# Kernel optimization log

Hardware: AMD Instinct MI355X
Metric: run time of the kernel (lower is better)

The kernel has to match this reference:

```python
import jax, jax.numpy as jnp
import numpy as np

HIDDEN = 2048
HEAD_DIM = 128
GROUPS = 8
HEADS = HIDDEN // HEAD_DIM          # 16
HPG = HEADS // GROUPS               # heads per group = 2


def setup_inputs() -> dict:
    key = jax.random.key(0)
    ks = jax.random.split(key, 9)
    b, sl, sk = 2, 2048, 2048
    s = 0.02
    return {
        "q": jax.random.normal(ks[0], (b, sl, HIDDEN), jnp.float32),
        "k": jax.random.normal(ks[1], (b, sk, HIDDEN), jnp.float32),
        "v": jax.random.normal(ks[2], (b, sk, HIDDEN), jnp.float32),
        "Wq": jax.random.normal(ks[3], (HIDDEN, HIDDEN), jnp.float32) * s,
        "bq": jax.random.normal(ks[4], (HIDDEN,), jnp.float32) * s,
        "Wk": jax.random.normal(ks[5], (HIDDEN, HEAD_DIM * GROUPS), jnp.float32) * s,
        "bk": jax.random.normal(ks[6], (HEAD_DIM * GROUPS,), jnp.float32) * s,
        "Wv": jax.random.normal(ks[7], (HIDDEN, HEAD_DIM * GROUPS), jnp.float32) * s,
        "bv": jax.random.normal(ks[8], (HEAD_DIM * GROUPS,), jnp.float32) * s,
    }


def reference(q, k, v, Wq, bq, Wk, bk, Wv, bv):
    b, sl, _ = q.shape
    sk = k.shape[1]
    qp = q @ Wq + bq                                   # [b, sl, hidden]
    kp = k @ Wk + bk                                   # [b, sk, G*d]
    vp = v @ Wv + bv                                   # [b, sk, G*d]
    # head h = g*HPG + j uses group g, matching torch repeat_interleave on dim=1
    qh = qp.reshape(b, sl, GROUPS, HPG, HEAD_DIM).transpose(0, 2, 3, 1, 4)  # [b,G,hpg,sl,d]
    kh = kp.reshape(b, sk, GROUPS, HEAD_DIM).transpose(0, 2, 1, 3)          # [b,G,sk,d]
    vh = vp.reshape(b, sk, GROUPS, HEAD_DIM).transpose(0, 2, 1, 3)          # [b,G,sk,d]
    scale = 1.0 / jnp.sqrt(jnp.asarray(HEAD_DIM, qh.dtype))
    score = jnp.einsum("bghld,bgsd->bghls", qh, kh) * scale                 # [b,G,hpg,sl,sk]
    attn = jax.nn.softmax(score, axis=-1)
    out = jnp.einsum("bghls,bgsd->bghld", attn, vh)                         # [b,G,hpg,sl,d]
    out = out.transpose(0, 3, 1, 2, 4).reshape(b, sl, HIDDEN)
    return out
```

## Files before the change

### kernel.cpp

```cpp
#include <hip/hip_runtime.h>

typedef unsigned short u16;
typedef short v8s __attribute__((ext_vector_type(8)));
typedef float v4f __attribute__((ext_vector_type(4)));
typedef float v16f __attribute__((ext_vector_type(16)));

typedef __attribute__((address_space(3))) u16* lptr_t;
typedef const __attribute__((address_space(1))) void* gptr_t;

__device__ __forceinline__ u16 f2b(float f) {
  unsigned int u = __float_as_uint(f);
  u += 0x7fff + ((u >> 16) & 1);
  return (u16)(u >> 16);
}

__global__ __launch_bounds__(256) void prep_all(const float* __restrict__ q,
                                                const float* __restrict__ k,
                                                const float* __restrict__ v,
                                                const float* __restrict__ Wq,
                                                const float* __restrict__ Wk,
                                                const float* __restrict__ Wv,
                                                u16* __restrict__ qd,
                                                u16* __restrict__ kd,
                                                u16* __restrict__ vd,
                                                u16* __restrict__ wt) {
  __shared__ u16 tile[64][65];
  int blk = blockIdx.x;
  if (blk < 12288) {
    const float* s; u16* d;
    if (blk < 4096)      { s = q; d = qd; }
    else if (blk < 8192) { s = k; d = kd; blk -= 4096; }
    else                 { s = v; d = vd; blk -= 8192; }
    int i = (blk * 256 + threadIdx.x) * 8;
    float4 a = *(const float4*)&s[i];
    float4 b = *(const float4*)&s[i + 4];
    union { uint4 v4; u16 u[8]; } p;
    p.u[0] = f2b(a.x); p.u[1] = f2b(a.y); p.u[2] = f2b(a.z); p.u[3] = f2b(a.w);
    p.u[4] = f2b(b.x); p.u[5] = f2b(b.y); p.u[6] = f2b(b.z); p.u[7] = f2b(b.w);
    *(uint4*)&d[i] = p.v4;
    return;
  }
  blk -= 12288;
  const float* W; int N; u16* dst;
  if (blk < 1024)      { W = Wq; N = 2048; dst = wt; }
  else if (blk < 1536) { W = Wk; N = 1024; dst = wt + (size_t)2048 * 2048; blk -= 1024; }
  else                 { W = Wv; N = 1024; dst = wt + (size_t)3072 * 2048; blk -= 1536; }
  const int k0 = (blk & 31) * 64;
  const int n0 = (blk >> 5) * 64;
  const int t = threadIdx.x;
#pragma unroll
  for (int i = 0; i < 2; ++i) {
    int chunk = i * 256 + t;
    int kr = chunk >> 3;
    int nc = (chunk & 7) * 8;
    float4 a = *(const float4*)&W[(size_t)(k0 + kr) * N + n0 + nc];
    float4 b = *(const float4*)&W[(size_t)(k0 + kr) * N + n0 + nc + 4];
    tile[kr][nc + 0] = f2b(a.x); tile[kr][nc + 1] = f2b(a.y);
    tile[kr][nc + 2] = f2b(a.z); tile[kr][nc + 3] = f2b(a.w);
    tile[kr][nc + 4] = f2b(b.x); tile[kr][nc + 5] = f2b(b.y);
    tile[kr][nc + 6] = f2b(b.z); tile[kr][nc + 7] = f2b(b.w);
  }
  __syncthreads();
#pragma unroll
  for (int i = 0; i < 2; ++i) {
    int chunk = i * 256 + t;
    int nr = chunk >> 3;
    int kc = (chunk & 7) * 8;
    union { uint4 v; u16 u[8]; } cv;
#pragma unroll
    for (int j = 0; j < 8; ++j) cv.u[j] = tile[kc + j][nr];
    *(uint4*)&dst[(size_t)(n0 + nr) * 2048 + k0 + kc] = cv.v;
  }
}

__global__ __launch_bounds__(512, 2) void qkv_gemm8(const u16* __restrict__ qbf,
                                                    const u16* __restrict__ kbf,
                                                    const u16* __restrict__ vbf,
                                                    const u16* __restrict__ wt_all,
                                                    const float* __restrict__ bq,
                                                    const float* __restrict__ bk,
                                                    const float* __restrict__ bv,
                                                    u16* __restrict__ qp,
                                                    u16* __restrict__ kp,
                                                    u16* __restrict__ vpt) {
  __shared__ __align__(16) u16 A_sh[2][16384];
  __shared__ __align__(16) u16 B_sh[2][16384];

  const int bid = blockIdx.x;
  const int wg = (bid & 7) * 32 + (bid >> 3);
  const int m0 = (wg >> 4) * 256;
  const int n0 = (wg & 15) * 256;

  const int t = threadIdx.x;
  const int w = t >> 6, lane = t & 63;
  const int quad = lane >> 4, l16 = lane & 15;
  const int wr = w >> 2, wc = w & 3;

  const u16* Abase; const float* bias; int region, nloc0;
  if (n0 < 2048)      { Abase = qbf; bias = bq; region = 0; nloc0 = n0; }
  else if (n0 < 3072) { Abase = kbf; bias = bk; region = 1; nloc0 = n0 - 2048; }
  else                { Abase = vbf; bias = bv; region = 2; nloc0 = n0 - 3072; }

  const u16* GA = Abase + (size_t)m0 * 2048;
  const u16* GB = wt_all + (size_t)n0 * 2048;

  int offA[2][2], ldsA[2][2], offB[2][2], ldsB[2][2];
#pragma unroll
  for (int s_ = 0; s_ < 2; ++s_)
#pragma unroll
    for (int j = 0; j < 2; ++j) {
      int r0a = j * 128 + s_ * 64 + w * 8;
      int ra = r0a + (lane >> 3);
      offA[s_][j] = ra * 2048 + (((lane & 7) ^ (ra & 7)) << 3);
      ldsA[s_][j] = r0a * 64 + lane * 8;
      int r0b = j * 128 + s_ * 32 + (w >> 2) * 64 + (w & 3) * 8;
      int rb = r0b + (lane >> 3);
      offB[s_][j] = rb * 2048 + (((lane & 7) ^ (rb & 7)) << 3);
      ldsB[s_][j] = r0b * 64 + lane * 8;
    }

  int colR[2];
#pragma unroll
  for (int kk = 0; kk < 2; ++kk)
    colR[kk] = ((kk * 4 + quad) ^ (l16 & 7)) << 3;

#define ST_A(BUF, KEL, S_)                                                              \
  do {                                                                                  \
    _Pragma("unroll") for (int j_ = 0; j_ < 2; ++j_) {                                  \
      const u16* g_ = GA + (KEL) + offA[S_][j_];                                        \
      lptr_t l_ = (lptr_t)&A_sh[BUF][ldsA[S_][j_]];                                     \
      __builtin_amdgcn_global_load_lds((gptr_t)g_,                                      \
                                       (__attribute__((address_space(3))) void*)l_,     \
                                       16, 0, 0);                                       \
    }                                                                                   \
  } while (0)

#define ST_B(BUF, KEL, S_)                                                              \
  do {                                                                                  \
    _Pragma("unroll") for (int j_ = 0; j_ < 2; ++j_) {                                  \
      const u16* g_ = GB + (KEL) + offB[S_][j_];                                        \
      lptr_t l_ = (lptr_t)&B_sh[BUF][ldsB[S_][j_]];                                     \
      __builtin_amdgcn_global_load_lds((gptr_t)g_,                                      \
                                       (__attribute__((address_space(3))) void*)l_,     \
                                       16, 0, 0);                                       \
    }                                                                                   \
  } while (0)

#define RD_A(BUF, MS, DST)                                                              \
  do {                                                                                  \
    const int rb_ = wr * 128 + (MS) * 64;                                               \
    _Pragma("unroll") for (int m_ = 0; m_ < 4; ++m_)                                    \
    _Pragma("unroll") for (int kk_ = 0; kk_ < 2; ++kk_)                                 \
      DST[m_][kk_] = *(const v8s*)&A_sh[BUF][(rb_ + m_ * 16 + l16) * 64 + colR[kk_]];   \
  } while (0)

#define RD_B(BUF, NS)                                                                   \
  do {                                                                                  \
    const int rb_ = wc * 64 + (NS) * 32;                                                \
    _Pragma("unroll") for (int n_ = 0; n_ < 2; ++n_)                                    \
    _Pragma("unroll") for (int kk_ = 0; kk_ < 2; ++kk_)                                 \
      b[n_][kk_] = *(const v8s*)&B_sh[BUF][(rb_ + n_ * 16 + l16) * 64 + colR[kk_]];     \
  } while (0)

#define MM(AR, MS, NS)                                                                  \
  do {                                                                                  \
    __builtin_amdgcn_s_setprio(1);                                                      \
    _Pragma("unroll") for (int kk_ = 0; kk_ < 2; ++kk_)                                 \
    _Pragma("unroll") for (int m_ = 0; m_ < 4; ++m_)                                    \
    _Pragma("unroll") for (int n_ = 0; n_ < 2; ++n_)                                    \
      acc[(MS) * 4 + m_][(NS) * 2 + n_] = __builtin_amdgcn_mfma_f32_16x16x32_bf16(      \
          AR[m_][kk_], b[n_][kk_], acc[(MS) * 4 + m_][(NS) * 2 + n_], 0, 0, 0);         \
    __builtin_amdgcn_s_setprio(0);                                                      \
  } while (0)

#define PHASE_MID()                                                                     \
  do {                                                                                  \
    asm volatile("" ::: "memory");                                                      \
    __builtin_amdgcn_s_barrier();                                                       \
    asm volatile("s_waitcnt lgkmcnt(0)" ::: "memory");                                  \
    __builtin_amdgcn_sched_barrier(0);                                                  \
  } while (0)

#define PHASE_END()                                                                     \
  do {                                                                                  \
    asm volatile("" ::: "memory");                                                      \
    __builtin_amdgcn_s_barrier();                                                       \
    __builtin_amdgcn_sched_barrier(0);                                                  \
  } while (0)

#define PHASE_END_V()                                                                   \
  do {                                                                                  \
    asm volatile("s_waitcnt vmcnt(6)" ::: "memory");                                    \
    __builtin_amdgcn_s_barrier();                                                       \
    __builtin_amdgcn_sched_barrier(0);                                                  \
  } while (0)

  v4f acc[8][4] = {};
  v8s a0[4][2], a1[4][2], b[2][2];

  ST_A(0, 0, 0); ST_B(0, 0, 0); ST_A(0, 0, 1); ST_B(0, 0, 1);
  ST_B(1, 64, 0); ST_A(1, 64, 1); ST_B(1, 64, 1);
  asm volatile("s_waitcnt vmcnt(6)" ::: "memory");
  __builtin_amdgcn_s_barrier();
  __builtin_amdgcn_sched_barrier(0);

  for (int it = 0; it < 16; ++it) {
    const int k1 = (2 * it + 1) * 64;
    const int k2 = ((2 * it + 2) & 31) * 64;
    const int k3 = ((2 * it + 3) & 31) * 64;
    RD_A(0, 0, a0); RD_B(0, 0); ST_A(1, k1, 0); PHASE_MID(); MM(a0, 0, 0); PHASE_END();
    RD_A(0, 1, a1);             ST_B(0, k2, 0); PHASE_MID(); MM(a1, 1, 0); PHASE_END();
    RD_B(0, 1);                 ST_A(0, k2, 1); PHASE_MID(); MM(a1, 1, 1); PHASE_END();
                                ST_B(0, k2, 1); PHASE_MID(); MM(a0, 0, 1); PHASE_END_V();
    RD_A(1, 0, a0); RD_B(1, 0); ST_A(0, k2, 0); PHASE_MID(); MM(a0, 0, 0); PHASE_END();
    RD_A(1, 1, a1);             ST_B(1, k3, 0); PHASE_MID(); MM(a1, 1, 0); PHASE_END();
    RD_B(1, 1);                 ST_A(1, k3, 1); PHASE_MID(); MM(a1, 1, 1); PHASE_END();
                                ST_B(1, k3, 1); PHASE_MID(); MM(a0, 0, 1); PHASE_END_V();
  }

#undef ST_A
#undef ST_B
#undef RD_A
#undef RD_B
#undef MM
#undef PHASE_MID
#undef PHASE_END
#undef PHASE_END_V

#pragma unroll
  for (int n = 0; n < 4; ++n) {
    int nl = nloc0 + wc * 64 + n * 16 + l16;
    float bvl = bias[nl];
    if (region == 0) {
#pragma unroll
      for (int m = 0; m < 8; ++m)
#pragma unroll
        for (int r = 0; r < 4; ++r) {
          int mg = m0 + wr * 128 + m * 16 + quad * 4 + r;
          qp[(size_t)mg * 2048 + nl] = f2b((acc[m][n][r] + bvl) * 0.12751744518608807f);
        }
    } else if (region == 1) {
#pragma unroll
      for (int m = 0; m < 8; ++m)
#pragma unroll
        for (int r = 0; r < 4; ++r) {
          int mg = m0 + wr * 128 + m * 16 + quad * 4 + r;
          kp[(size_t)mg * 1024 + nl] = f2b(acc[m][n][r] + bvl);
        }
    } else {
      int g = nl >> 7, d = nl & 127;
#pragma unroll
      for (int m = 0; m < 8; ++m) {
        int mb = m0 + wr * 128 + m * 16 + quad * 4;
        int bb = mb >> 11, s = mb & 2047;
        ushort4 pk;
        pk.x = f2b(acc[m][n][0] + bvl);
        pk.y = f2b(acc[m][n][1] + bvl);
        pk.z = f2b(acc[m][n][2] + bvl);
        pk.w = f2b(acc[m][n][3] + bvl);
        *(ushort4*)&vpt[(((size_t)bb * 8 + g) * 128 + d) * 2048 + s] = pk;
      }
    }
  }
}

__global__ __launch_bounds__(256, 2) void gqa_attn2(const u16* __restrict__ qp,
                                                    const u16* __restrict__ kp,
                                                    const u16* __restrict__ vpt,
                                                    float* __restrict__ out) {
  __shared__ __align__(16) u16 K_sh[2][64 * 128];
  __shared__ __align__(16) u16 V_sh[2][128 * 64];

  const int qtile = blockIdx.x;
  const int head = blockIdx.y;
  const int batch = blockIdx.z;
  const int g = head >> 1;
  const int q0 = qtile * 128;

  const u16* qpb = qp + (size_t)batch * 2048 * 2048;
  const u16* kpb = kp + (size_t)batch * 2048 * 1024;
  const u16* vptb = vpt + (size_t)batch * 8 * 128 * 2048;
  float* outb = out + (size_t)batch * 2048 * 2048;

  const int t = threadIdx.x;
  const int wave = t >> 6, lane = t & 63;
  const int l = lane & 31, h = lane >> 5;

  v8s qf[8];
  {
    const u16* qrow = &qpb[(size_t)(q0 + wave * 32 + l) * 2048 + head * 128];
#pragma unroll
    for (int ks = 0; ks < 8; ++ks)
      qf[ks] = *(const v8s*)&qrow[ks * 16 + h * 8];
  }

  int colK[8];
#pragma unroll
  for (int ks = 0; ks < 8; ++ks) colK[ks] = ((2 * ks + h) ^ (l & 7)) * 8;

  int koff[4], voff[4];
#pragma unroll
  for (int i = 0; i < 4; ++i) {
    int krow = wave * 16 + i * 4 + (lane >> 4);
    int kg = (lane & 15) ^ (krow & 7);
    koff[i] = krow * 1024 + g * 128 + kg * 8;
    int vrow = wave * 32 + i * 8 + (lane >> 3);
    int vg = (lane & 7) ^ (vrow & 7);
    voff[i] = (g * 128 + vrow) * 2048 + vg * 8;
  }

#define STAGE_KV(BUF, S0)                                                               \
  do {                                                                                  \
    _Pragma("unroll") for (int i_ = 0; i_ < 4; ++i_) {                                  \
      const u16* gk_ = kpb + (size_t)(S0) * 1024 + koff[i_];                            \
      lptr_t lk_ = (lptr_t)&K_sh[BUF][(wave * 16 + i_ * 4) * 128] + lane * 8;           \
      __builtin_amdgcn_global_load_lds((gptr_t)gk_,                                     \
                                       (__attribute__((address_space(3))) void*)lk_,    \
                                       16, 0, 0);                                       \
      const u16* gv_ = vptb + voff[i_] + (S0);                                          \
      lptr_t lv_ = (lptr_t)&V_sh[BUF][(wave * 32 + i_ * 8) * 64] + lane * 8;            \
      __builtin_amdgcn_global_load_lds((gptr_t)gv_,                                     \
                                       (__attribute__((address_space(3))) void*)lv_,    \
                                       16, 0, 0);                                       \
    }                                                                                   \
  } while (0)

  v16f o_acc[4] = {};
  float rs = 0.0f;

  STAGE_KV(0, 0);
  __syncthreads();

  int cur = 0;
  for (int sc = 0; sc < 32; ++sc) {
    if (sc < 31) STAGE_KV(cur ^ 1, (sc + 1) * 64);

    v16f s0a = {}, s0b = {}, s1a = {}, s1b = {};
    __builtin_amdgcn_s_setprio(1);
#pragma unroll
    for (int ks = 0; ks < 4; ++ks) {
      v8s kf0 = *(const v8s*)&K_sh[cur][l * 128 + colK[ks]];
      s0a = __builtin_amdgcn_mfma_f32_32x32x16_bf16(kf0, qf[ks], s0a, 0, 0, 0);
      v8s kf1 = *(const v8s*)&K_sh[cur][(32 + l) * 128 + colK[ks]];
      s1a = __builtin_amdgcn_mfma_f32_32x32x16_bf16(kf1, qf[ks], s1a, 0, 0, 0);
    }
#pragma unroll
    for (int ks = 4; ks < 8; ++ks) {
      v8s kf0 = *(const v8s*)&K_sh[cur][l * 128 + colK[ks]];
      s0b = __builtin_amdgcn_mfma_f32_32x32x16_bf16(kf0, qf[ks], s0b, 0, 0, 0);
      v8s kf1 = *(const v8s*)&K_sh[cur][(32 + l) * 128 + colK[ks]];
      s1b = __builtin_amdgcn_mfma_f32_32x32x16_bf16(kf1, qf[ks], s1b, 0, 0, 0);
    }
    __builtin_amdgcn_s_setprio(0);

    v16f sacc[2];
    sacc[0] = s0a + s0b;
    sacc[1] = s1a + s1b;

    unsigned int wv[16];
#pragma unroll
    for (int kb = 0; kb < 2; ++kb)
#pragma unroll
      for (int p = 0; p < 8; ++p) {
        float e0 = __builtin_amdgcn_exp2f(sacc[kb][2 * p]);
        float e1 = __builtin_amdgcn_exp2f(sacc[kb][2 * p + 1]);
        rs += e0 + e1;
        asm("v_cvt_pk_bf16_f32 %0, %1, %2" : "=v"(wv[kb * 8 + p]) : "v"(e0), "v"(e1));
      }

    v8s pa[4];
#pragma unroll
    for (int j = 0; j < 4; ++j) {
      unsigned int a = wv[j * 4 + 0], c = wv[j * 4 + 1];
      unsigned int b = wv[j * 4 + 2], d = wv[j * 4 + 3];
      asm("v_permlane32_swap_b32 %0, %1" : "+v"(a), "+v"(b));
      asm("v_permlane32_swap_b32 %0, %1" : "+v"(c), "+v"(d));
      union { unsigned int u[4]; v8s s; } pk;
      pk.u[0] = a; pk.u[1] = c; pk.u[2] = b; pk.u[3] = d;
      pa[j] = pk.s;
    }

    __builtin_amdgcn_s_setprio(1);
#pragma unroll
    for (int j = 0; j < 4; ++j)
#pragma unroll
      for (int db = 0; db < 4; ++db) {
        v8s vf = *(const v8s*)&V_sh[cur][(db * 32 + l) * 64 + colK[j]];
        o_acc[db] = __builtin_amdgcn_mfma_f32_32x32x16_bf16(pa[j], vf, o_acc[db], 0, 0, 0);
      }
    __builtin_amdgcn_s_setprio(0);

    __syncthreads();
    cur ^= 1;
  }

  float rst = rs + __shfl_xor(rs, 32, 64);
  float inv = 1.0f / rst;
#pragma unroll
  for (int r = 0; r < 16; ++r) {
    int qpat = (r & 3) + 8 * (r >> 2) + 4 * h;
    float invq = __shfl(inv, qpat, 64);
    int qrow = q0 + wave * 32 + qpat;
    float* orow = &outb[(size_t)qrow * 2048 + head * 128 + l];
#pragma unroll
    for (int db = 0; db < 4; ++db)
      orow[db * 32] = o_acc[db][r] * invq;
  }
#undef STAGE_KV
}

extern "C" void kernel_launch(void* const* d_in, const int* in_sizes, int n_in,
                              void* d_out, int out_size, void* d_ws, size_t ws_size,
                              hipStream_t stream) {
  const float* q  = (const float*)d_in[0];
  const float* k  = (const float*)d_in[1];
  const float* v  = (const float*)d_in[2];
  const float* Wq = (const float*)d_in[3];
  const float* bq = (const float*)d_in[4];
  const float* Wk = (const float*)d_in[5];
  const float* bk = (const float*)d_in[6];
  const float* Wv = (const float*)d_in[7];
  const float* bv = (const float*)d_in[8];
  float* out = (float*)d_out;
  char* ws = (char*)d_ws;

  u16* qbf    = (u16*)(ws + 0);
  u16* kbf    = (u16*)(ws + 16777216);
  u16* vbf    = (u16*)(ws + 33554432);
  u16* wt_all = (u16*)(ws + 50331648);
  u16* qp     = (u16*)(ws + 67108864);
  u16* kp     = (u16*)(ws + 83886080);
  u16* vpt    = (u16*)(ws + 92274688);

  prep_all<<<14336, 256, 0, stream>>>(q, k, v, Wq, Wk, Wv, qbf, kbf, vbf, wt_all);
  qkv_gemm8<<<256, 512, 0, stream>>>(qbf, kbf, vbf, wt_all,
                                     bq, bk, bv, qp, kp, vpt);
  gqa_attn2<<<dim3(16, 16, 2), 256, 0, stream>>>(qp, kp, vpt, out);
}
```

Baseline: 320.6 us.

## Split attention KV range across two wave groups and reduce partials in LDS

The attention kernel now uses 512 threads per block. Two groups of four waves each process half of the key/value sequence for the same query tile, and the two partial outputs and row sums are then combined through shared memory. The aim is more waves per block and more latency hiding. In exchange, the double-buffered prefetch is dropped: each group loads its tile and then synchronises before computing, so loads no longer overlap compute, and an extra LDS reduction epilogue is added.

```diff
diff --git a/kernel.cpp b/kernel.cpp
--- a/kernel.cpp
+++ b/kernel.cpp
@@ -264,7 +264,7 @@
   }
 }
 
-__global__ __launch_bounds__(256, 2) void gqa_attn2(const u16* __restrict__ qp,
+__global__ __launch_bounds__(512, 2) void gqa_attn4(const u16* __restrict__ qp,
                                                     const u16* __restrict__ kp,
                                                     const u16* __restrict__ vpt,
                                                     float* __restrict__ out) {
@@ -284,11 +284,13 @@
 
   const int t = threadIdx.x;
   const int wave = t >> 6, lane = t & 63;
+  const int kh = wave >> 2;
+  const int w4 = wave & 3;
   const int l = lane & 31, h = lane >> 5;
 
   v8s qf[8];
   {
-    const u16* qrow = &qpb[(size_t)(q0 + wave * 32 + l) * 2048 + head * 128];
+    const u16* qrow = &qpb[(size_t)(q0 + w4 * 32 + l) * 2048 + head * 128];
 #pragma unroll
     for (int ks = 0; ks < 8; ++ks)
       qf[ks] = *(const v8s*)&qrow[ks * 16 + h * 8];
@@ -301,54 +303,49 @@
   int koff[4], voff[4];
 #pragma unroll
   for (int i = 0; i < 4; ++i) {
-    int krow = wave * 16 + i * 4 + (lane >> 4);
+    int krow = w4 * 16 + i * 4 + (lane >> 4);
     int kg = (lane & 15) ^ (krow & 7);
     koff[i] = krow * 1024 + g * 128 + kg * 8;
-    int vrow = wave * 32 + i * 8 + (lane >> 3);
+    int vrow = w4 * 32 + i * 8 + (lane >> 3);
     int vg = (lane & 7) ^ (vrow & 7);
     voff[i] = (g * 128 + vrow) * 2048 + vg * 8;
   }
 
-#define STAGE_KV(BUF, S0)                                                               \
-  do {                                                                                  \
-    _Pragma("unroll") for (int i_ = 0; i_ < 4; ++i_) {                                  \
-      const u16* gk_ = kpb + (size_t)(S0) * 1024 + koff[i_];                            \
-      lptr_t lk_ = (lptr_t)&K_sh[BUF][(wave * 16 + i_ * 4) * 128] + lane * 8;           \
-      __builtin_amdgcn_global_load_lds((gptr_t)gk_,                                     \
-                                       (__attribute__((address_space(3))) void*)lk_,    \
-                                       16, 0, 0);                                       \
-      const u16* gv_ = vptb + voff[i_] + (S0);                                          \
-      lptr_t lv_ = (lptr_t)&V_sh[BUF][(wave * 32 + i_ * 8) * 64] + lane * 8;            \
-      __builtin_amdgcn_global_load_lds((gptr_t)gv_,                                     \
-                                       (__attribute__((address_space(3))) void*)lv_,    \
-                                       16, 0, 0);                                       \
-    }                                                                                   \
-  } while (0)
-
   v16f o_acc[4] = {};
   float rs = 0.0f;
 
-  STAGE_KV(0, 0);
-  __syncthreads();
-
-  int cur = 0;
-  for (int sc = 0; sc < 32; ++sc) {
-    if (sc < 31) STAGE_KV(cur ^ 1, (sc + 1) * 64);
+  for (int sc = 0; sc < 16; ++sc) {
+    const int s0 = (kh * 16 + sc) * 64;
+
+#pragma unroll
+    for (int i_ = 0; i_ < 4; ++i_) {
+      const u16* gk_ = kpb + (size_t)s0 * 1024 + koff[i_];
+      lptr_t lk_ = (lptr_t)&K_sh[kh][(w4 * 16 + i_ * 4) * 128] + lane * 8;
+      __builtin_amdgcn_global_load_lds((gptr_t)gk_,
+                                       (__attribute__((address_space(3))) void*)lk_,
+                                       16, 0, 0);
+      const u16* gv_ = vptb + voff[i_] + s0;
+      lptr_t lv_ = (lptr_t)&V_sh[kh][(w4 * 32 + i_ * 8) * 64] + lane * 8;
+      __builtin_amdgcn_global_load_lds((gptr_t)gv_,
+                                       (__attribute__((address_space(3))) void*)lv_,
+                                       16, 0, 0);
+    }
+    __syncthreads();
 
     v16f s0a = {}, s0b = {}, s1a = {}, s1b = {};
     __builtin_amdgcn_s_setprio(1);
 #pragma unroll
     for (int ks = 0; ks < 4; ++ks) {
-      v8s kf0 = *(const v8s*)&K_sh[cur][l * 128 + colK[ks]];
+      v8s kf0 = *(const v8s*)&K_sh[kh][l * 128 + colK[ks]];
       s0a = __builtin_amdgcn_mfma_f32_32x32x16_bf16(kf0, qf[ks], s0a, 0, 0, 0);
-      v8s kf1 = *(const v8s*)&K_sh[cur][(32 + l) * 128 + colK[ks]];
+      v8s kf1 = *(const v8s*)&K_sh[kh][(32 + l) * 128 + colK[ks]];
       s1a = __builtin_amdgcn_mfma_f32_32x32x16_bf16(kf1, qf[ks], s1a, 0, 0, 0);
     }
 #pragma unroll
     for (int ks = 4; ks < 8; ++ks) {
-      v8s kf0 = *(const v8s*)&K_sh[cur][l * 128 + colK[ks]];
+      v8s kf0 = *(const v8s*)&K_sh[kh][l * 128 + colK[ks]];
       s0b = __builtin_amdgcn_mfma_f32_32x32x16_bf16(kf0, qf[ks], s0b, 0, 0, 0);
-      v8s kf1 = *(const v8s*)&K_sh[cur][(32 + l) * 128 + colK[ks]];
+      v8s kf1 = *(const v8s*)&K_sh[kh][(32 + l) * 128 + colK[ks]];
       s1b = __builtin_amdgcn_mfma_f32_32x32x16_bf16(kf1, qf[ks], s1b, 0, 0, 0);
     }
     __builtin_amdgcn_s_setprio(0);
@@ -385,28 +382,64 @@
     for (int j = 0; j < 4; ++j)
 #pragma unroll
       for (int db = 0; db < 4; ++db) {
-        v8s vf = *(const v8s*)&V_sh[cur][(db * 32 + l) * 64 + colK[j]];
+        v8s vf = *(const v8s*)&V_sh[kh][(db * 32 + l) * 64 + colK[j]];
         o_acc[db] = __builtin_amdgcn_mfma_f32_32x32x16_bf16(pa[j], vf, o_acc[db], 0, 0, 0);
       }
     __builtin_amdgcn_s_setprio(0);
 
     __syncthreads();
-    cur ^= 1;
-  }
-
-  float rst = rs + __shfl_xor(rs, 32, 64);
-  float inv = 1.0f / rst;
-#pragma unroll
-  for (int r = 0; r < 16; ++r) {
-    int qpat = (r & 3) + 8 * (r >> 2) + 4 * h;
-    float invq = __shfl(inv, qpat, 64);
-    int qrow = q0 + wave * 32 + qpat;
-    float* orow = &outb[(size_t)qrow * 2048 + head * 128 + l];
-#pragma unroll
-    for (int db = 0; db < 4; ++db)
-      orow[db * 32] = o_acc[db][r] * invq;
-  }
-#undef STAGE_KV
+  }
+
+  float* scr = (float*)&K_sh[0][0];
+  float* scr2 = (float*)&V_sh[0][0];
+  const int slot = (w4 * 64 + lane) * 32;
+
+  if (kh == 1) {
+    scr2[w4 * 64 + lane] = rs;
+#pragma unroll
+    for (int db = 0; db < 2; ++db)
+#pragma unroll
+      for (int r = 0; r < 16; ++r)
+        scr[slot + db * 16 + r] = o_acc[db][r];
+  }
+  __syncthreads();
+  if (kh == 0) {
+    rs += scr2[w4 * 64 + lane];
+#pragma unroll
+    for (int db = 0; db < 2; ++db)
+#pragma unroll
+      for (int r = 0; r < 16; ++r)
+        o_acc[db][r] += scr[slot + db * 16 + r];
+  }
+  __syncthreads();
+  if (kh == 1) {
+#pragma unroll
+    for (int db = 2; db < 4; ++db)
+#pragma unroll
+      for (int r = 0; r < 16; ++r)
+        scr[slot + (db - 2) * 16 + r] = o_acc[db][r];
+  }
+  __syncthreads();
+  if (kh == 0) {
+#pragma unroll
+    for (int db = 2; db < 4; ++db)
+#pragma unroll
+      for (int r = 0; r < 16; ++r)
+        o_acc[db][r] += scr[slot + (db - 2) * 16 + r];
+
+    float rst = rs + __shfl_xor(rs, 32, 64);
+    float inv = 1.0f / rst;
+#pragma unroll
+    for (int r = 0; r < 16; ++r) {
+      int qpat = (r & 3) + 8 * (r >> 2) + 4 * h;
+      float invq = __shfl(inv, qpat, 64);
+      int qrow = q0 + w4 * 32 + qpat;
+      float* orow = &outb[(size_t)qrow * 2048 + head * 128 + l];
+#pragma unroll
+      for (int db = 0; db < 4; ++db)
+        orow[db * 32] = o_acc[db][r] * invq;
+    }
+  }
 }
 
 extern "C" void kernel_launch(void* const* d_in, const int* in_sizes, int n_in,
@@ -435,5 +468,5 @@
   prep_all<<<14336, 256, 0, stream>>>(q, k, v, Wq, Wk, Wv, qbf, kbf, vbf, wt_all);
   qkv_gemm8<<<256, 512, 0, stream>>>(qbf, kbf, vbf, wt_all,
                                      bq, bk, bv, qp, kp, vpt);
-  gqa_attn2<<<dim3(16, 16, 2), 256, 0, stream>>>(qp, kp, vpt, out);
+  gqa_attn4<<<dim3(16, 16, 2), 512, 0, stream>>>(qp, kp, vpt, out);
 }
```

After: 343.0 us. 7.0% more time.
